# Kernel tuning notes

Hardware: AMD Instinct MI355X
Metric: run time of the kernel (lower is better)

The kernel has to match this reference:

```python
import jax, jax.numpy as jnp
import numpy as np

TAGSET = 5
START = 3  # tag_to_ix['<START>']
STOP = 4   # tag_to_ix['<STOP>']
NEG_INF = -10000.0


def setup_inputs() -> dict:
    key = jax.random.key(0)
    ks = jax.random.split(key, 12)
    T, V, E, H = 4096, 50000, 1024, 512  # seq_len, vocab, embed_dim, per-direction hidden
    scale = 0.02
    sentence = jax.random.randint(ks[0], (T,), 0, V)
    embed = jax.random.normal(ks[1], (V, E), jnp.float32) * scale
    W_ih_f = jax.random.normal(ks[2], (4 * H, E), jnp.float32) * scale
    W_hh_f = jax.random.normal(ks[3], (4 * H, H), jnp.float32) * scale
    b_f = jnp.zeros((4 * H,), jnp.float32)
    W_ih_b = jax.random.normal(ks[4], (4 * H, E), jnp.float32) * scale
    W_hh_b = jax.random.normal(ks[5], (4 * H, H), jnp.float32) * scale
    b_b = jnp.zeros((4 * H,), jnp.float32)
    h0 = jax.random.normal(ks[6], (2, H), jnp.float32) * scale
    c0 = jax.random.normal(ks[7], (2, H), jnp.float32) * scale
    W_out = jax.random.normal(ks[8], (TAGSET, 2 * H), jnp.float32) * scale
    b_out = jnp.zeros((TAGSET,), jnp.float32)
    transitions = jax.random.normal(ks[9], (TAGSET, TAGSET), jnp.float32)
    transitions = transitions.at[START, :].set(NEG_INF).at[:, STOP].set(NEG_INF)
    return dict(sentence=sentence, embed=embed, W_ih_f=W_ih_f, W_hh_f=W_hh_f, b_f=b_f,
                W_ih_b=W_ih_b, W_hh_b=W_hh_b, b_b=b_b, h0=h0, c0=c0,
                W_out=W_out, b_out=b_out, transitions=transitions)


def _lstm_dir(x, W_ih, W_hh, b, h0, c0):
    # x: [T, E]; single-layer LSTM, PyTorch gate order i,f,g,o
    def step(carry, xt):
        h, c = carry
        gates = W_ih @ xt + W_hh @ h + b  # [4H]
        i, f, g, o = jnp.split(gates, 4)
        i = jax.nn.sigmoid(i)
        f = jax.nn.sigmoid(f)
        g = jnp.tanh(g)
        o = jax.nn.sigmoid(o)
        c = f * c + i * g
        h = o * jnp.tanh(c)
        return (h, c), h
    _, hs = jax.lax.scan(step, (h0, c0), x)
    return hs  # [T, H]


def reference(sentence, embed, W_ih_f, W_hh_f, b_f, W_ih_b, W_hh_b, b_b, h0, c0, W_out, b_out, transitions):
    # BiLSTM features
    x = embed[sentence]                       # [T, E]
    hf = _lstm_dir(x, W_ih_f, W_hh_f, b_f, h0[0], c0[0])
    hb = _lstm_dir(x[::-1], W_ih_b, W_hh_b, b_b, h0[1], c0[1])[::-1]
    feats = jnp.concatenate([hf, hb], axis=-1) @ W_out.T + b_out  # [T, 5]

    # Viterbi decode
    init = jnp.full((TAGSET,), NEG_INF, feats.dtype).at[START].set(0.0)

    def vstep(fv, feat):
        scores = fv[None, :] + transitions    # [next_tag, prev_tag]
        bp = jnp.argmax(scores, axis=1)       # backpointers
        fv_new = jnp.max(scores, axis=1) + feat
        return fv_new, bp

    fv, bptrs = jax.lax.scan(vstep, init, feats)  # bptrs: [T, 5]
    terminal = fv + transitions[STOP]
    best_last = jnp.argmax(terminal)
    score = jnp.max(terminal)

    # Backtrack: original uses rows T-1 .. 1 of the backpointer table
    def back(y, bp):
        prev = bp[y]
        return prev, prev
    _, rev = jax.lax.scan(back, best_last, bptrs[1:][::-1])
    path = jnp.concatenate([rev[::-1], best_last[None]])  # [T], tag ids in order
    return score, path
```

## Files before the change

kernel.cpp:

```cpp
#include <hip/hip_runtime.h>
#include <hip/hip_bf16.h>


#define T_LEN 4096
#define EDIM  1024
#define HID   512
#define G4    2048

typedef short short8 __attribute__((ext_vector_type(8)));
typedef float f32x4  __attribute__((ext_vector_type(4)));

__device__ __forceinline__ float bf16_to_f32(unsigned bits) {
  return __uint_as_float(bits << 16);
}
__device__ __forceinline__ unsigned bf16rne(float f) {
  unsigned u = __float_as_uint(f);
  return (u + 0x7fffu + ((u >> 16) & 1u)) >> 16;
}

__device__ __forceinline__ float wave_sum64(float x) {
  int t;
  t = __builtin_amdgcn_update_dpp(0, __float_as_int(x), 0x111, 0xf, 0xf, true); x += __int_as_float(t);
  t = __builtin_amdgcn_update_dpp(0, __float_as_int(x), 0x112, 0xf, 0xf, true); x += __int_as_float(t);
  t = __builtin_amdgcn_update_dpp(0, __float_as_int(x), 0x114, 0xf, 0xf, true); x += __int_as_float(t);
  t = __builtin_amdgcn_update_dpp(0, __float_as_int(x), 0x118, 0xf, 0xf, true); x += __int_as_float(t);
  t = __builtin_amdgcn_update_dpp(0, __float_as_int(x), 0x142, 0xf, 0xf, true); x += __int_as_float(t);
  t = __builtin_amdgcn_update_dpp(0, __float_as_int(x), 0x143, 0xf, 0xf, true); x += __int_as_float(t);
  return x;
}

__device__ __forceinline__ float fsig(float x) {
  return __builtin_amdgcn_rcpf(1.f + __builtin_amdgcn_exp2f(-1.44269504f * x));
}
__device__ __forceinline__ float ftanh(float x) {
  return 1.f - 2.f * __builtin_amdgcn_rcpf(1.f + __builtin_amdgcn_exp2f(2.88539008f * x));
}

__global__ __launch_bounds__(256) void gather_kernel(
    const int* __restrict__ sent, const float* __restrict__ embed,
    unsigned short* __restrict__ xbf)
{
  const int t = blockIdx.x;
  const int tok = sent[t];
  const int e = threadIdx.x * 4;
  const float4 v = *(const float4*)(embed + (size_t)tok * EDIM + e);
  uint2 o;
  o.x = bf16rne(v.x) | (bf16rne(v.y) << 16);
  o.y = bf16rne(v.z) | (bf16rne(v.w) << 16);
  *(uint2*)(xbf + (size_t)t * EDIM + e) = o;
}

__global__ __launch_bounds__(256) void convw_kernel(
    const float* __restrict__ Wf, const float* __restrict__ Wb,
    unsigned short* __restrict__ of, unsigned short* __restrict__ ob)
{
  const float* src = blockIdx.z ? Wb : Wf;
  unsigned short* dst = blockIdx.z ? ob : of;
  const size_t idx = (size_t)blockIdx.x * 2048 + (size_t)threadIdx.x * 8;
  const float4 a = *(const float4*)(src + idx);
  const float4 b = *(const float4*)(src + idx + 4);
  uint4 o;
  o.x = bf16rne(a.x) | (bf16rne(a.y) << 16);
  o.y = bf16rne(a.z) | (bf16rne(a.w) << 16);
  o.z = bf16rne(b.x) | (bf16rne(b.y) << 16);
  o.w = bf16rne(b.z) | (bf16rne(b.w) << 16);
  *(uint4*)(dst + idx) = o;
}

__global__ __launch_bounds__(512) void inith_kernel(
    const float* __restrict__ h0, unsigned* __restrict__ hcF,
    unsigned* __restrict__ hcB)
{
  unsigned* hc = blockIdx.x ? hcB : hcF;
  const int j = threadIdx.x;
  hc[j] = bf16rne(h0[blockIdx.x * HID + j]);
}

__global__ __launch_bounds__(256) void gemm_x_kernel(
    const unsigned short* __restrict__ xbf,
    const unsigned short* __restrict__ Wfb, const unsigned short* __restrict__ Wbb,
    const float* __restrict__ biasF, const float* __restrict__ biasB,
    float* __restrict__ Xf, float* __restrict__ Xb)
{
  const int zz = blockIdx.z;
  const unsigned short* Bp = zz ? Wbb : Wfb;
  const float* bias = zz ? biasB : biasF;
  float* C = zz ? Xb : Xf;
  const int n0 = blockIdx.x * 64;
  const int m0 = blockIdx.y * 64;
  __shared__ unsigned short As[64][40];
  __shared__ unsigned short Bs[64][40];
  const int tid = threadIdx.x;
  const int wv = tid >> 6, lane = tid & 63;
  const int moff = (wv >> 1) * 32, noff = (wv & 1) * 32;
  const int lrow = tid >> 2, lseg = (tid & 3) * 8;
  const int fr = lane & 15;
  const int fk = (lane >> 4) * 8;
  f32x4 acc[2][2];
#pragma unroll
  for (int i = 0; i < 2; i++)
#pragma unroll
    for (int j = 0; j < 2; j++) acc[i][j] = (f32x4){0.f, 0.f, 0.f, 0.f};

  for (int k0 = 0; k0 < EDIM; k0 += 32) {
    const uint4 av = *(const uint4*)(xbf + (size_t)(m0 + lrow) * EDIM + k0 + lseg);
    const uint4 bv = *(const uint4*)(Bp  + (size_t)(n0 + lrow) * EDIM + k0 + lseg);
    *(uint4*)&As[lrow][lseg] = av;
    *(uint4*)&Bs[lrow][lseg] = bv;
    __syncthreads();
    short8 af[2], bg[2];
#pragma unroll
    for (int i = 0; i < 2; i++) af[i] = *(const short8*)&As[moff + i * 16 + fr][fk];
#pragma unroll
    for (int j = 0; j < 2; j++) bg[j] = *(const short8*)&Bs[noff + j * 16 + fr][fk];
#pragma unroll
    for (int i = 0; i < 2; i++)
#pragma unroll
      for (int j = 0; j < 2; j++)
        acc[i][j] = __builtin_amdgcn_mfma_f32_16x16x32_bf16(af[i], bg[j], acc[i][j], 0, 0, 0);
    __syncthreads();
  }
#pragma unroll
  for (int i = 0; i < 2; i++)
#pragma unroll
    for (int j = 0; j < 2; j++) {
      const int col = n0 + noff + j * 16 + fr;
      const float bv = bias[col];
#pragma unroll
      for (int r = 0; r < 4; r++) {
        const int row = m0 + moff + i * 16 + (lane >> 4) * 4 + r;
        C[(size_t)row * G4 + col] = acc[i][j][r] + bv;
      }
    }
}

__global__ __launch_bounds__(512) void lstm_kernel(
    const float* __restrict__ WhhF, const float* __restrict__ WhhB,
    const float* __restrict__ Xf, const float* __restrict__ Xb,
    const float* __restrict__ c0,
    unsigned* __restrict__ hcF, unsigned* __restrict__ hcB)
{
  const int b = blockIdx.x;
  const int dir = b >> 5;
  const float* Whh = dir ? WhhB : WhhF;
  const float* X   = dir ? Xb : Xf;
  unsigned* hcomm  = dir ? hcB : hcF;

  const int tid = threadIdx.x;
  const int w = tid >> 6;
  const int c = tid & 63;
  const int jw = (b & 31) * 16 + 2 * w;

  __shared__ float hl[2][HID];
  __shared__ int flg[2][8];

  float4 wA[8], wB[8];
#pragma unroll
  for (int g = 0; g < 4; ++g)
#pragma unroll
    for (int p = 0; p < 2; ++p) {
      const float* row = Whh + (size_t)(g * HID + jw + p) * HID;
      wA[g * 2 + p] = *(const float4*)(row + 4 * c);
      wB[g * 2 + p] = *(const float4*)(row + 256 + 4 * c);
    }

  if (tid < 16) ((int*)flg)[tid] = -1;
  __syncthreads();

  float cs0 = 0.f, cs1 = 0.f;
  float2 xc[4], xn[4];
#pragma unroll
  for (int g = 0; g < 4; ++g) { xc[g] = make_float2(0.f, 0.f); xn[g] = make_float2(0.f, 0.f); }
  if (c == 63) {
    cs0 = c0[dir * HID + jw];
    cs1 = c0[dir * HID + jw + 1];
    const int xrow0 = dir ? (T_LEN - 1) : 0;
#pragma unroll
    for (int g = 0; g < 4; ++g)
      xc[g] = *(const float2*)(X + (size_t)xrow0 * G4 + g * HID + jw);
  }

  for (int s = 0; s < T_LEN; ++s) {
    if (c == 63 && s + 1 < T_LEN) {
      const int xrow = dir ? (T_LEN - 2 - s) : (s + 1);
#pragma unroll
      for (int g = 0; g < 4; ++g)
        xn[g] = *(const float2*)(X + (size_t)xrow * G4 + g * HID + jw);
    }

    const unsigned want = (unsigned)s;
    float* hbuf = hl[s & 1];
    volatile int* fl = flg[s & 1];

    {
      const unsigned* ap = hcomm + (size_t)s * HID + w * 64 + c;
      unsigned v;
      for (;;) {
        v = __hip_atomic_load(ap, __ATOMIC_RELAXED, __HIP_MEMORY_SCOPE_AGENT);
        if (__all((int)((v >> 16) == want))) break;
      }
      hbuf[w * 64 + c] = bf16_to_f32(v & 0xffffu);
      asm volatile("s_waitcnt lgkmcnt(0)" ::: "memory");
      if (c == 0) fl[w] = (int)s;
    }
    for (;;) {
      const int fv = fl[c & 7];
      if (__all(fv == (int)s)) break;
    }

    const float4 hA = *(const float4*)&hbuf[4 * c];
    const float4 hB = *(const float4*)&hbuf[256 + 4 * c];
    float sum[8];
#pragma unroll
    for (int r = 0; r < 8; ++r) {
      float sr = wA[r].x * hA.x + wA[r].y * hA.y + wA[r].z * hA.z + wA[r].w * hA.w
               + wB[r].x * hB.x + wB[r].y * hB.y + wB[r].z * hB.z + wB[r].w * hB.w;
      sum[r] = wave_sum64(sr);
    }

    if (c == 63) {
      const float i0 = fsig (sum[0] + xc[0].x), i1 = fsig (sum[1] + xc[0].y);
      const float f0 = fsig (sum[2] + xc[1].x), f1 = fsig (sum[3] + xc[1].y);
      const float g0 = ftanh(sum[4] + xc[2].x), g1 = ftanh(sum[5] + xc[2].y);
      const float o0 = fsig (sum[6] + xc[3].x), o1 = fsig (sum[7] + xc[3].y);
      cs0 = f0 * cs0 + i0 * g0;
      cs1 = f1 * cs1 + i1 * g1;
      const float h0v = o0 * ftanh(cs0);
      const float h1v = o1 * ftanh(cs1);
      const unsigned tag = (unsigned)(s + 1) << 16;
      const unsigned long long pk =
          ((unsigned long long)(tag | bf16rne(h1v)) << 32) | (tag | bf16rne(h0v));
      __hip_atomic_store((unsigned long long*)(hcomm + (size_t)(s + 1) * HID + jw), pk,
                         __ATOMIC_RELAXED, __HIP_MEMORY_SCOPE_AGENT);
    }
#pragma unroll
    for (int g = 0; g < 4; ++g) xc[g] = xn[g];
  }
}

__global__ __launch_bounds__(320) void feats_kernel(
    const unsigned* __restrict__ hcF, const unsigned* __restrict__ hcB,
    const float* __restrict__ Wout, const float* __restrict__ bout,
    float* __restrict__ feats)
{
  const int t = blockIdx.x;
  const int tag = threadIdx.x >> 6;
  const int lane = threadIdx.x & 63;
  const unsigned* hf = hcF + (size_t)(t + 1) * HID;
  const unsigned* hb = hcB + (size_t)(T_LEN - t) * HID;
  float sum = 0.f;
  for (int e = lane; e < HID; e += 64) {
    sum += Wout[tag * 1024 + e]       * bf16_to_f32(hf[e] & 0xffffu);
    sum += Wout[tag * 1024 + 512 + e] * bf16_to_f32(hb[e] & 0xffffu);
  }
#pragma unroll
  for (int m = 1; m < 64; m <<= 1) sum += __shfl_xor(sum, m, 64);
  if (lane == 0) feats[t * 5 + tag] = sum + bout[tag];
}

__device__ __forceinline__ unsigned map_compose(unsigned a, unsigned b) {
  unsigned r = 0;
#pragma unroll
  for (int i = 0; i < 5; ++i) {
    const unsigned gi = (b >> (3 * i)) & 7u;
    r |= ((a >> (3 * gi)) & 7u) << (3 * i);
  }
  return r;
}

__global__ __launch_bounds__(64) void viterbi_kernel(
    const float* __restrict__ feats, const float* __restrict__ trans,
    float* __restrict__ out)
{
  __shared__ float fe[2][2560];
  __shared__ unsigned char bpb[5][T_LEN];
  const int lane = threadIdx.x;
  const int n = lane >> 3, p = lane & 7;
  const bool act = (n < 5) && (p < 5);
  const int nn = (n < 5) ? n : 0;
  const float tr = act ? trans[n * 5 + p] : -3.0e38f;
  float fvp = (p == 3) ? 0.f : -10000.f;

  for (int i = lane; i < 2560; i += 64) fe[0][i] = feats[i];
  __syncthreads();

  for (int ch = 0; ch < 8; ++ch) {
    const int buf = ch & 1;
    float pf[40];
    if (ch < 7) {
#pragma unroll
      for (int i = 0; i < 40; ++i)
        pf[i] = feats[(ch + 1) * 2560 + i * 64 + lane];
    }
    for (int tt = 0; tt < 512; ++tt) {
      const int t = ch * 512 + tt;
      float s = act ? (fvp + tr) : -3.0e38f;
      float bm = s; int bp_ = p;
#pragma unroll
      for (int d = 1; d < 8; d <<= 1) {
        const float os = __shfl_xor(bm, d, 64);
        const int   op = __shfl_xor(bp_, d, 64);
        if (os > bm || (os == bm && op < bp_)) { bm = os; bp_ = op; }
      }
      const float fvn = bm + fe[buf][tt * 5 + nn];
      if (p == 0 && n < 5) bpb[n][t] = (unsigned char)bp_;
      fvp = __shfl(fvn, p * 8, 64);
    }
    __syncthreads();
    if (ch < 7) {
#pragma unroll
      for (int i = 0; i < 40; ++i) fe[buf ^ 1][i * 64 + lane] = pf[i];
    }
    __syncthreads();
  }

  float tv = (lane < 5) ? (fvp + trans[4 * 5 + lane]) : -3.0e38f;
  int bl = lane;
#pragma unroll
  for (int d = 1; d < 8; d <<= 1) {
    const float ov = __shfl_xor(tv, d, 64);
    const int   ol = __shfl_xor(bl, d, 64);
    if (ov > tv || (ov == tv && ol < bl)) { tv = ov; bl = ol; }
  }
  const float score = __shfl(tv, 0, 64);
  const int best = __shfl(bl, 0, 64);
  if (lane == 0) out[0] = score;

  const unsigned IDENT = 0u | (1u << 3) | (2u << 6) | (3u << 9) | (4u << 12);
  const int lo = lane * 64;
  unsigned msave[64];
  unsigned comp = IDENT;
#pragma unroll
  for (int tt = 0; tt < 64; ++tt) {
    const int t = lo + tt;
    unsigned mt;
    if (t == 0) mt = IDENT;
    else
      mt = (unsigned)bpb[0][t] | ((unsigned)bpb[1][t] << 3) |
           ((unsigned)bpb[2][t] << 6) | ((unsigned)bpb[3][t] << 9) |
           ((unsigned)bpb[4][t] << 12);
    msave[tt] = mt;
    comp = map_compose(comp, mt);
  }
  unsigned inc = comp;
#pragma unroll
  for (int d = 1; d < 64; d <<= 1) {
    const unsigned other = __shfl_down(inc, d, 64);
    const unsigned comb = map_compose(inc, other);
    if (lane + d < 64) inc = comb;
  }
  unsigned exc = __shfl_down(inc, 1, 64);
  if (lane == 63) exc = IDENT;

  int y = (int)((exc >> (3 * best)) & 7u);
  out[1 + lo + 63] = (float)y;
#pragma unroll
  for (int tt = 63; tt >= 0; --tt) {
    const int t = lo + tt;
    if (t == 0) break;
    y = (int)((msave[tt] >> (3 * y)) & 7u);
    out[1 + t - 1] = (float)y;
  }
}

extern "C" void kernel_launch(void* const* d_in, const int* in_sizes, int n_in,
                              void* d_out, int out_size, void* d_ws, size_t ws_size,
                              hipStream_t stream) {
  const int*   sent   = (const int*)d_in[0];
  const float* embed  = (const float*)d_in[1];
  const float* W_ih_f = (const float*)d_in[2];
  const float* W_hh_f = (const float*)d_in[3];
  const float* b_f    = (const float*)d_in[4];
  const float* W_ih_b = (const float*)d_in[5];
  const float* W_hh_b = (const float*)d_in[6];
  const float* b_b    = (const float*)d_in[7];
  const float* h0     = (const float*)d_in[8];
  const float* c0     = (const float*)d_in[9];
  const float* W_out  = (const float*)d_in[10];
  const float* b_out  = (const float*)d_in[11];
  const float* trans  = (const float*)d_in[12];

  char* ws = (char*)d_ws;
  float*          Xf    = (float*)(ws + 0);
  float*          Xb    = (float*)(ws + 33554432);
  unsigned short* xbf   = (unsigned short*)(ws + 67108864);
  unsigned short* Wfb   = (unsigned short*)(ws + 75497472);
  unsigned short* Wbb   = (unsigned short*)(ws + 79691776);
  unsigned*       hcF   = (unsigned*)(ws + 83886080);
  unsigned*       hcB   = (unsigned*)(ws + 92276736);
  float*          feats = (float*)(ws + 100667392);
  float*          out   = (float*)d_out;

  gather_kernel<<<T_LEN, 256, 0, stream>>>(sent, embed, xbf);
  convw_kernel<<<dim3(1024, 1, 2), 256, 0, stream>>>(W_ih_f, W_ih_b, Wfb, Wbb);
  inith_kernel<<<2, 512, 0, stream>>>(h0, hcF, hcB);
  gemm_x_kernel<<<dim3(32, 64, 2), 256, 0, stream>>>(xbf, Wfb, Wbb, b_f, b_b, Xf, Xb);
  lstm_kernel<<<64, 512, 0, stream>>>(W_hh_f, W_hh_b, Xf, Xb, c0, hcF, hcB);
  feats_kernel<<<T_LEN, 320, 0, stream>>>(hcF, hcB, W_out, b_out, feats);
  viterbi_kernel<<<1, 64, 0, stream>>>(feats, trans, out);
}
```

Before: 11.50 ms.

## Add XCD-local fast h-exchange path with adaptive slow-path fallback in LSTM

The grid becomes 256 blocks, and the block index is mapped so that each direction's 32 working blocks land on one XCD (bid&7 selects the direction), with the rest exiting at once. Each step's h is stored to a second buffer with sc0 (non-coherent, L2-local) stores and polled with sc0 loads, which aims to cut the cross-die coherent-memory latency of the per-step barrier. The old agent-scope buffer is still written, sometimes deferred and polled less often once the fast path hits, so feats_kernel still sees correct data. The scheme relies on the round-robin block-to-XCD mapping and reuses workspace regions (xbf/Wfb) as the fast buffers, so it depends on undocumented placement and adds polling complexity.

```diff
diff --git a/kernel.cpp b/kernel.cpp
--- a/kernel.cpp
+++ b/kernel.cpp
@@ -138,18 +138,23 @@
     const float* __restrict__ WhhF, const float* __restrict__ WhhB,
     const float* __restrict__ Xf, const float* __restrict__ Xb,
     const float* __restrict__ c0,
-    unsigned* __restrict__ hcF, unsigned* __restrict__ hcB)
-{
-  const int b = blockIdx.x;
-  const int dir = b >> 5;
+    unsigned* __restrict__ hcF, unsigned* __restrict__ hcB,
+    unsigned* __restrict__ hfF, unsigned* __restrict__ hfB)
+{
+  const int bid = blockIdx.x;
+  const int dir = bid & 7;
+  const int slot = bid >> 3;
+  if (dir >= 2 || slot >= 32) return;
+
   const float* Whh = dir ? WhhB : WhhF;
   const float* X   = dir ? Xb : Xf;
   unsigned* hcomm  = dir ? hcB : hcF;
+  unsigned* hfast  = dir ? hfB : hfF;
 
   const int tid = threadIdx.x;
   const int w = tid >> 6;
   const int c = tid & 63;
-  const int jw = (b & 31) * 16 + 2 * w;
+  const int jw = slot * 16 + 2 * w;
 
   __shared__ float hl[2][HID];
   __shared__ int flg[2][8];
@@ -180,29 +185,74 @@
       xc[g] = *(const float2*)(X + (size_t)xrow0 * G4 + g * HID + jw);
   }
 
+  int kslow = 1;
+  bool spend = false;
+  unsigned long long pk_pend = 0;
+
   for (int s = 0; s < T_LEN; ++s) {
-    if (c == 63 && s + 1 < T_LEN) {
-      const int xrow = dir ? (T_LEN - 2 - s) : (s + 1);
-#pragma unroll
-      for (int g = 0; g < 4; ++g)
-        xn[g] = *(const float2*)(X + (size_t)xrow * G4 + g * HID + jw);
-    }
-
     const unsigned want = (unsigned)s;
     float* hbuf = hl[s & 1];
     volatile int* fl = flg[s & 1];
-
-    {
-      const unsigned* ap = hcomm + (size_t)s * HID + w * 64 + c;
-      unsigned v;
+    const int base = (w << 6) + c;
+    unsigned* spst = hcomm + (size_t)s * HID + jw;
+
+    unsigned v = 0;
+
+    if (s == 0) {
+      const unsigned* ap = hcomm + base;
       for (;;) {
         v = __hip_atomic_load(ap, __ATOMIC_RELAXED, __HIP_MEMORY_SCOPE_AGENT);
         if (__all((int)((v >> 16) == want))) break;
       }
-      hbuf[w * 64 + c] = bf16_to_f32(v & 0xffffu);
-      asm volatile("s_waitcnt lgkmcnt(0)" ::: "memory");
-      if (c == 0) fl[w] = (int)s;
-    }
+    } else {
+      const unsigned* fp = hfast + (size_t)(s - 1) * HID + base;
+      const unsigned* sp = hcomm + (size_t)s * HID + base;
+      int it = 0, ms = 0;
+      bool fast_hit = false;
+      for (;;) {
+        ++it;
+        unsigned vf;
+        if (++ms >= kslow) {
+          ms = 0;
+          asm volatile("global_load_dword %0, %1, off sc0" : "=v"(vf) : "v"(fp) : "memory");
+          unsigned vs = __hip_atomic_load(sp, __ATOMIC_RELAXED, __HIP_MEMORY_SCOPE_AGENT);
+          asm volatile("s_waitcnt vmcnt(0)" ::: "memory");
+          __builtin_amdgcn_sched_barrier(0);
+          if (__all((int)((vf >> 16) == want))) { v = vf; fast_hit = true; break; }
+          const unsigned vm = ((vf >> 16) == want) ? vf : vs;
+          if (__all((int)((vm >> 16) == want))) { v = vm; break; }
+        } else {
+          asm volatile("global_load_dword %0, %1, off sc0" : "=v"(vf) : "v"(fp) : "memory");
+          asm volatile("s_waitcnt vmcnt(0)" ::: "memory");
+          __builtin_amdgcn_sched_barrier(0);
+          if (__all((int)((vf >> 16) == want))) { v = vf; fast_hit = true; break; }
+        }
+        if (spend && it >= 8) {
+          if (c == 63)
+            __hip_atomic_store((unsigned long long*)spst, pk_pend,
+                               __ATOMIC_RELAXED, __HIP_MEMORY_SCOPE_AGENT);
+          spend = false;
+        }
+      }
+      kslow = fast_hit ? 16 : 1;
+    }
+
+    if (spend) {
+      if (c == 63)
+        __hip_atomic_store((unsigned long long*)spst, pk_pend,
+                           __ATOMIC_RELAXED, __HIP_MEMORY_SCOPE_AGENT);
+      spend = false;
+    }
+    if (c == 63 && s + 1 < T_LEN) {
+      const int xrow = dir ? (T_LEN - 2 - s) : (s + 1);
+#pragma unroll
+      for (int g = 0; g < 4; ++g)
+        xn[g] = *(const float2*)(X + (size_t)xrow * G4 + g * HID + jw);
+    }
+
+    hbuf[base] = bf16_to_f32(v & 0xffffu);
+    asm volatile("s_waitcnt lgkmcnt(0)" ::: "memory");
+    if (c == 0) fl[w] = (int)s;
     for (;;) {
       const int fv = fl[c & 7];
       if (__all(fv == (int)s)) break;
@@ -230,12 +280,22 @@
       const unsigned tag = (unsigned)(s + 1) << 16;
       const unsigned long long pk =
           ((unsigned long long)(tag | bf16rne(h1v)) << 32) | (tag | bf16rne(h0v));
-      __hip_atomic_store((unsigned long long*)(hcomm + (size_t)(s + 1) * HID + jw), pk,
-                         __ATOMIC_RELAXED, __HIP_MEMORY_SCOPE_AGENT);
-    }
+      unsigned* fdst = hfast + (size_t)s * HID + jw;
+      asm volatile("global_store_dwordx2 %0, %1, off sc0" :: "v"(fdst), "v"(pk) : "memory");
+      pk_pend = pk;
+      if (kslow == 1) {
+        __hip_atomic_store((unsigned long long*)(hcomm + (size_t)(s + 1) * HID + jw), pk,
+                           __ATOMIC_RELAXED, __HIP_MEMORY_SCOPE_AGENT);
+      }
+    }
+    spend = (kslow != 1);
 #pragma unroll
     for (int g = 0; g < 4; ++g) xc[g] = xn[g];
   }
+
+  if (spend && c == 63)
+    __hip_atomic_store((unsigned long long*)(hcomm + (size_t)T_LEN * HID + jw), pk_pend,
+                       __ATOMIC_RELAXED, __HIP_MEMORY_SCOPE_AGENT);
 }
 
 __global__ __launch_bounds__(320) void feats_kernel(
@@ -389,13 +449,15 @@
   unsigned*       hcF   = (unsigned*)(ws + 83886080);
   unsigned*       hcB   = (unsigned*)(ws + 92276736);
   float*          feats = (float*)(ws + 100667392);
+  unsigned*       hfF   = (unsigned*)(ws + 67108864);
+  unsigned*       hfB   = (unsigned*)(ws + 75497472);
   float*          out   = (float*)d_out;
 
   gather_kernel<<<T_LEN, 256, 0, stream>>>(sent, embed, xbf);
   convw_kernel<<<dim3(1024, 1, 2), 256, 0, stream>>>(W_ih_f, W_ih_b, Wfb, Wbb);
   inith_kernel<<<2, 512, 0, stream>>>(h0, hcF, hcB);
   gemm_x_kernel<<<dim3(32, 64, 2), 256, 0, stream>>>(xbf, Wfb, Wbb, b_f, b_b, Xf, Xb);
-  lstm_kernel<<<64, 512, 0, stream>>>(W_hh_f, W_hh_b, Xf, Xb, c0, hcF, hcB);
+  lstm_kernel<<<256, 512, 0, stream>>>(W_hh_f, W_hh_b, Xf, Xb, c0, hcF, hcB, hfF, hfB);
   feats_kernel<<<T_LEN, 320, 0, stream>>>(hcF, hcB, W_out, b_out, feats);
   viterbi_kernel<<<1, 64, 0, stream>>>(feats, trans, out);
 }
```

Result: slower. 24.81 ms (+115.7%).

## Add dedicated publisher wave and speculative prefetch of next-step hidden state

Applied to the files above, without the earlier changes.

Adds a ninth wave per LSTM block that gathers the 16 new hidden values from LDS staging and publishes them to global memory with coalesced atomic stores, replacing the per-wave 64-bit stores. Compute waves also issue a coherent (sc0 sc1) load of the next step's h slot right after the local barrier, and use it directly if its tags already match. This is meant to shorten the cross-block handoff latency on the serial recurrence. It costs an extra wave, more LDS flag polling, and a wasted load whenever the speculative value arrives stale.

```diff
diff --git a/kernel.cpp b/kernel.cpp
--- a/kernel.cpp
+++ b/kernel.cpp
@@ -134,7 +134,7 @@
     }
 }
 
-__global__ __launch_bounds__(512) void lstm_kernel(
+__global__ __launch_bounds__(576) void lstm_kernel(
     const float* __restrict__ WhhF, const float* __restrict__ WhhB,
     const float* __restrict__ Xf, const float* __restrict__ Xb,
     const float* __restrict__ c0,
@@ -149,10 +149,36 @@
   const int tid = threadIdx.x;
   const int w = tid >> 6;
   const int c = tid & 63;
-  const int jw = (b & 31) * 16 + 2 * w;
+  const int blk16 = (b & 31) * 16;
+  const int jw = blk16 + 2 * w;
 
   __shared__ float hl[2][HID];
   __shared__ int flg[2][8];
+  __shared__ unsigned hstage[2][16];
+  __shared__ int gflg[2][8];
+
+  if (tid < 16) ((int*)flg)[tid] = -1;
+  else if (tid < 32) ((int*)gflg)[tid - 16] = -1;
+  __syncthreads();
+
+  if (w == 8) {
+    for (int s = 0; s < T_LEN; ++s) {
+      const int par = (s + 1) & 1;
+      volatile int* gfl = gflg[par];
+      for (;;) {
+        const int fv = gfl[c & 7];
+        if (__all(fv == (int)s)) break;
+      }
+      asm volatile("" ::: "memory");
+      if (c < 16) {
+        const unsigned val = ((volatile unsigned*)hstage[par])[c];
+        __hip_atomic_store(hcomm + (size_t)(s + 1) * HID + blk16 + c, val,
+                           __ATOMIC_RELAXED, __HIP_MEMORY_SCOPE_AGENT);
+      }
+    }
+    asm volatile("s_waitcnt vmcnt(0)" ::: "memory");
+    return;
+  }
 
   float4 wA[8], wB[8];
 #pragma unroll
@@ -163,9 +189,6 @@
       wA[g * 2 + p] = *(const float4*)(row + 4 * c);
       wB[g * 2 + p] = *(const float4*)(row + 256 + 4 * c);
     }
-
-  if (tid < 16) ((int*)flg)[tid] = -1;
-  __syncthreads();
 
   float cs0 = 0.f, cs1 = 0.f;
   float2 xc[4], xn[4];
@@ -180,32 +203,44 @@
       xc[g] = *(const float2*)(X + (size_t)xrow0 * G4 + g * HID + jw);
   }
 
+  unsigned pre = 0;
+
   for (int s = 0; s < T_LEN; ++s) {
-    if (c == 63 && s + 1 < T_LEN) {
-      const int xrow = dir ? (T_LEN - 2 - s) : (s + 1);
-#pragma unroll
-      for (int g = 0; g < 4; ++g)
-        xn[g] = *(const float2*)(X + (size_t)xrow * G4 + g * HID + jw);
-    }
-
     const unsigned want = (unsigned)s;
     float* hbuf = hl[s & 1];
     volatile int* fl = flg[s & 1];
-
-    {
-      const unsigned* ap = hcomm + (size_t)s * HID + w * 64 + c;
-      unsigned v;
+    const unsigned* ap = hcomm + (size_t)s * HID + (w << 6) + c;
+    unsigned v;
+
+    asm volatile("s_waitcnt vmcnt(0)" ::: "memory");
+    __builtin_amdgcn_sched_barrier(0);
+    if (s > 0 && __all((int)((pre >> 16) == want))) {
+      v = pre;
+    } else {
       for (;;) {
         v = __hip_atomic_load(ap, __ATOMIC_RELAXED, __HIP_MEMORY_SCOPE_AGENT);
         if (__all((int)((v >> 16) == want))) break;
       }
-      hbuf[w * 64 + c] = bf16_to_f32(v & 0xffffu);
-      asm volatile("s_waitcnt lgkmcnt(0)" ::: "memory");
-      if (c == 0) fl[w] = (int)s;
-    }
+    }
+
+    hbuf[(w << 6) + c] = bf16_to_f32(v & 0xffffu);
+    asm volatile("s_waitcnt lgkmcnt(0)" ::: "memory");
+    if (c == 0) fl[w] = (int)s;
     for (;;) {
       const int fv = fl[c & 7];
       if (__all(fv == (int)s)) break;
+    }
+    asm volatile("" ::: "memory");
+
+    if (s + 1 < T_LEN) {
+      const unsigned* apn = ap + HID;
+      asm volatile("global_load_dword %0, %1, off sc0 sc1" : "=v"(pre) : "v"(apn) : "memory");
+      if (c == 63) {
+        const int xrow = dir ? (T_LEN - 2 - s) : (s + 1);
+#pragma unroll
+        for (int g = 0; g < 4; ++g)
+          xn[g] = *(const float2*)(X + (size_t)xrow * G4 + g * HID + jw);
+      }
     }
 
     const float4 hA = *(const float4*)&hbuf[4 * c];
@@ -228,14 +263,17 @@
       const float h0v = o0 * ftanh(cs0);
       const float h1v = o1 * ftanh(cs1);
       const unsigned tag = (unsigned)(s + 1) << 16;
-      const unsigned long long pk =
-          ((unsigned long long)(tag | bf16rne(h1v)) << 32) | (tag | bf16rne(h0v));
-      __hip_atomic_store((unsigned long long*)(hcomm + (size_t)(s + 1) * HID + jw), pk,
-                         __ATOMIC_RELAXED, __HIP_MEMORY_SCOPE_AGENT);
+      volatile unsigned* st = hstage[(s + 1) & 1];
+      st[2 * w]     = tag | bf16rne(h0v);
+      st[2 * w + 1] = tag | bf16rne(h1v);
+      asm volatile("s_waitcnt lgkmcnt(0)" ::: "memory");
+      ((volatile int*)gflg[(s + 1) & 1])[w] = (int)s;
     }
 #pragma unroll
     for (int g = 0; g < 4; ++g) xc[g] = xn[g];
-  }
+    asm volatile("" : "+v"(pre));
+  }
+  asm volatile("s_waitcnt vmcnt(0)" ::: "memory");
 }
 
 __global__ __launch_bounds__(320) void feats_kernel(
@@ -395,7 +433,7 @@
   convw_kernel<<<dim3(1024, 1, 2), 256, 0, stream>>>(W_ih_f, W_ih_b, Wfb, Wbb);
   inith_kernel<<<2, 512, 0, stream>>>(h0, hcF, hcB);
   gemm_x_kernel<<<dim3(32, 64, 2), 256, 0, stream>>>(xbf, Wfb, Wbb, b_f, b_b, Xf, Xb);
-  lstm_kernel<<<64, 512, 0, stream>>>(W_hh_f, W_hh_b, Xf, Xb, c0, hcF, hcB);
+  lstm_kernel<<<64, 576, 0, stream>>>(W_hh_f, W_hh_b, Xf, Xb, c0, hcF, hcB);
   feats_kernel<<<T_LEN, 320, 0, stream>>>(hcF, hcB, W_out, b_out, feats);
   viterbi_kernel<<<1, 64, 0, stream>>>(feats, trans, out);
 }
```

Measured after the change: 9.510 ms. 17.3% less time.
